# Kernel optimization log

Hardware: AMD Instinct MI355X
Metric: run time of the kernel (lower is better)

The kernel has to match this reference:

```python
import jax, jax.numpy as jnp
import numpy as np

N = 100_000   # nodes
E = 640_000   # edges
H = 128       # hidden_dim
L = 4         # num_layers
C = 2         # num_classes
G = 128       # graphs in batch

def setup_inputs() -> dict:
    key = jax.random.key(0)
    ks = jax.random.split(key, 8)
    x = jax.random.randint(ks[0], (N, 1), 0, 2)
    edge_index = jax.random.randint(ks[1], (2, E), 0, N)
    batch = jnp.sort(jax.random.randint(ks[2], (N,), 0, G))
    embed = jax.random.normal(ks[3], (2, H), jnp.float32)
    Ws = jax.random.normal(ks[4], (L, H, H), jnp.float32) * (1.0 / np.sqrt(H))
    bs = jnp.zeros((L, H), jnp.float32)
    W_out = jax.random.normal(ks[5], (H, C), jnp.float32) * (1.0 / np.sqrt(H))
    b_out = jnp.zeros((C,), jnp.float32)
    return dict(x=x, edge_index=edge_index, batch=batch, embed=embed,
                Ws=Ws, bs=bs, W_out=W_out, b_out=b_out)

def reference(x, edge_index, batch, embed, Ws, bs, W_out, b_out):
    src, dst = edge_index[0], edge_index[1]
    # symmetric GCN normalization with self-loops (PyG GCNConv default)
    deg = jax.ops.segment_sum(jnp.ones(E, jnp.float32), dst, num_segments=N) + 1.0
    dinv = jax.lax.rsqrt(deg)
    enorm = (dinv[src] * dinv[dst])[:, None]   # per-edge norm
    snorm = (dinv * dinv)[:, None]             # self-loop norm

    h = embed[x[:, 0]]                          # [N, H] embedding lookup
    n_layers = Ws.shape[0]
    for l in range(n_layers):
        t = h @ Ws[l]                           # linear transform [N, H]
        agg = jax.ops.segment_sum(t[src] * enorm, dst, num_segments=N) \
              + t * snorm + bs[l]
        h = jax.nn.relu(agg) if l < n_layers - 1 else agg

    # global mean pool over graph ids
    counts = jax.ops.segment_sum(jnp.ones(N, jnp.float32), batch, num_segments=G)
    pooled = jax.ops.segment_sum(h, batch, num_segments=G) \
             / jnp.maximum(counts, 1.0)[:, None]   # [G, H]
    return pooled @ W_out + b_out                  # [G, C]
```

## Files before the change

### kernel.cpp

```cpp
#include <hip/hip_runtime.h>

typedef __attribute__((ext_vector_type(8))) short bf16x8;
typedef __attribute__((ext_vector_type(4))) float f32x4;
typedef __attribute__((ext_vector_type(2))) float f32x2;

__device__ inline unsigned short bf16_rtn(float f) {
  unsigned u = __float_as_uint(f);
  unsigned r = u + 0x7fffu + ((u >> 16) & 1u);
  return (unsigned short)(r >> 16);
}

__device__ inline void split_bf16(float f, unsigned short& hi, unsigned short& lo) {
  hi = bf16_rtn(f);
  float fh = __uint_as_float((unsigned)hi << 16);
  lo = bf16_rtn(f - fh);
}

__device__ inline float bf16_to_f(unsigned short v) {
  return __uint_as_float((unsigned)v << 16);
}

__device__ inline unsigned char f_to_fp8(float f) {
  int r = __builtin_amdgcn_cvt_pk_fp8_f32(f, f, 0, false);
  return (unsigned char)(r & 0xff);
}
__device__ inline f32x2 fp8x2_to_f(unsigned short v) {
  return __builtin_amdgcn_cvt_pk_f32_fp8((int)v, false);
}

__global__ void k_init(int* __restrict__ deg, int* __restrict__ gpz, int N, int M,
                       const float* __restrict__ Ws, const float* __restrict__ embed,
                       unsigned short* __restrict__ wphi,
                       unsigned short* __restrict__ wplo,
                       float* __restrict__ T,
                       unsigned char* __restrict__ t_a,
                       unsigned char* __restrict__ t_b) {
  int i = blockIdx.x * 256 + threadIdx.x;
  if (i < N) deg[i] = 0;
  if (i < M) gpz[i] = 0;
  int l = blockIdx.x;
  if (l < 3) {
    const float* W = Ws + (size_t)(l + 1) * 128 * 128;
    unsigned short* dh = wphi + (size_t)l * 16384;
    unsigned short* dl = wplo + (size_t)l * 16384;
    for (int idx = threadIdx.x; idx < 16384; idx += 256) {
      int j = idx & 7;
      int lane = (idx >> 3) & 63;
      int c = (idx >> 9) & 3;
      int ct = idx >> 11;
      int k = c * 32 + ((lane >> 4) * 8) + j;
      int n = ct * 16 + (lane & 15);
      unsigned short hi, lo;
      split_bf16(W[k * 128 + n], hi, lo);
      dh[idx] = hi;
      dl[idx] = lo;
    }
  } else if (l == 3) {
    int t = threadIdx.x;
    int r = t >> 7, c = t & 127;
    float acc = 0.f;
    for (int k = 0; k < 128; ++k)
      acc += embed[r * 128 + k] * Ws[k * 128 + c];
    T[r * 128 + c] = acc;
  } else if (l == 4) {
    int t = threadIdx.x;
    if (t < 32)      ((unsigned*)(t_a + (size_t)N * 128))[t] = 0u;
    else if (t < 64) ((unsigned*)(t_b + (size_t)N * 128))[t - 32] = 0u;
  }
}


__global__ void k_hist(const int* __restrict__ dst, int* __restrict__ deg,
                       int* __restrict__ posr, int E) {
  int e = blockIdx.x * 256 + threadIdx.x;
  if (e < E) posr[e] = atomicAdd(&deg[dst[e]], 1);
}

__global__ void k_scan1(const int* __restrict__ deg, int* __restrict__ rowptr,
                        int* __restrict__ bsum, float* __restrict__ dpk,
                        const int* __restrict__ x, const int* __restrict__ batch,
                        int* __restrict__ gstart, int* __restrict__ gend, int N) {
  __shared__ int s[256];
  int t = threadIdx.x;
  int i = blockIdx.x * 256 + t;
  int v = (i < N) ? deg[i] : 0;
  if (i < N) {
    float di = rsqrtf((float)v + 1.0f);
    dpk[i] = x[i] ? -di : di;
    int g = batch[i];
    if (i == 0 || batch[i - 1] != g) gstart[g] = i;
    if (i == N - 1 || batch[i + 1] != g) gend[g] = i + 1;
  }
  s[t] = v;
  __syncthreads();
  for (int off = 1; off < 256; off <<= 1) {
    int u = (t >= off) ? s[t - off] : 0;
    __syncthreads();
    s[t] += u;
    __syncthreads();
  }
  if (i < N) rowptr[i] = s[t] - v;
  if (t == 255) bsum[blockIdx.x] = s[255];
}

__global__ void k_scan2(const int* __restrict__ bsum, int* __restrict__ boff, int nb) {
  __shared__ int s[512];
  int t = threadIdx.x;
  int v = (t < nb) ? bsum[t] : 0;
  s[t] = v;
  __syncthreads();
  for (int off = 1; off < 512; off <<= 1) {
    int u = (t >= off) ? s[t - off] : 0;
    __syncthreads();
    s[t] += u;
    __syncthreads();
  }
  boff[t] = s[t] - v;
}

__global__ void k_scan3(int* __restrict__ rowptr, const int* __restrict__ boff,
                        int N, int E) {
  int i = blockIdx.x * 256 + threadIdx.x;
  if (i < N) rowptr[i] += boff[i >> 8];
  if (i == 0) rowptr[N] = E;
}

__global__ void k_scatter(const int* __restrict__ src, const int* __restrict__ dst,
                          const int* __restrict__ posr, const int* __restrict__ rowptr,
                          const float* __restrict__ dpk,
                          int2* __restrict__ epack, int E) {
  int e = blockIdx.x * 256 + threadIdx.x;
  if (e >= E) return;
  int s = src[e], d = dst[e];
  int pos = rowptr[d] + posr[e];
  epack[pos] = make_int2(s, __float_as_int(dpk[s]));
}


__device__ inline void acc16(float* a, uint4 p) {
  f32x2 v;
  v = __builtin_amdgcn_cvt_pk_f32_fp8((int)p.x, false); a[0]  += v.x; a[1]  += v.y;
  v = __builtin_amdgcn_cvt_pk_f32_fp8((int)p.x, true);  a[2]  += v.x; a[3]  += v.y;
  v = __builtin_amdgcn_cvt_pk_f32_fp8((int)p.y, false); a[4]  += v.x; a[5]  += v.y;
  v = __builtin_amdgcn_cvt_pk_f32_fp8((int)p.y, true);  a[6]  += v.x; a[7]  += v.y;
  v = __builtin_amdgcn_cvt_pk_f32_fp8((int)p.z, false); a[8]  += v.x; a[9]  += v.y;
  v = __builtin_amdgcn_cvt_pk_f32_fp8((int)p.z, true);  a[10] += v.x; a[11] += v.y;
  v = __builtin_amdgcn_cvt_pk_f32_fp8((int)p.w, false); a[12] += v.x; a[13] += v.y;
  v = __builtin_amdgcn_cvt_pk_f32_fp8((int)p.w, true);  a[14] += v.x; a[15] += v.y;
}

__device__ inline void gather8(const unsigned char* __restrict__ tin,
                               const int2* __restrict__ epack,
                               int r0, int deg, int l8, int N,
                               float* a) {
  int dcap = deg < 16 ? deg : 16;
  int slo = N, shi = N;
  if (2 * l8 < dcap)     slo = epack[r0 + 2 * l8].x;
  if (2 * l8 + 1 < dcap) shi = epack[r0 + 2 * l8 + 1].x;

  uint4 p[16];
  #pragma unroll
  for (int k = 0; k < 8; ++k) {
    int se = __shfl(slo, k, 8);
    int so = __shfl(shi, k, 8);
    p[2 * k]     = *(const uint4*)(tin + (size_t)((unsigned)se * 128u + ((unsigned)l8 << 4)));
    p[2 * k + 1] = *(const uint4*)(tin + (size_t)((unsigned)so * 128u + ((unsigned)l8 << 4)));
  }
  #pragma unroll
  for (int k = 0; k < 16; ++k) acc16(a, p[k]);

  if (__builtin_expect(deg > 16, 0)) {
    for (int e = r0 + 16; e < r0 + deg; ++e) {
      int s = epack[e].x;
      uint4 q = *(const uint4*)(tin + (size_t)((unsigned)s * 128u + ((unsigned)l8 << 4)));
      acc16(a, q);
    }
  }
}

__global__ __launch_bounds__(256)
void k_agg(const unsigned char* __restrict__ tin,
           const int* __restrict__ rowptr,
           const int2* __restrict__ epack,
           const float* __restrict__ dpk, const float* __restrict__ bvec,
           unsigned short* __restrict__ h, int N) {
  int lane = threadIdx.x & 63;
  int g8 = lane >> 3, l8 = lane & 7;
  int wid = (blockIdx.x * 256 + threadIdx.x) >> 6;
  int i = wid * 8 + g8;
  if (i >= N) return;
  int r0 = rowptr[i], r1 = rowptr[i + 1];
  uint4 ps = *(const uint4*)(tin + (size_t)i * 128 + (l8 << 4));
  float dp = dpk[i];

  float a[16];
  #pragma unroll
  for (int k = 0; k < 16; ++k) a[k] = 0.f;
  gather8(tin, epack, r0, r1 - r0, l8, N, a);
  acc16(a, ps);

  float di = fabsf(dp);
  const float4* bp = (const float4*)(bvec + 16 * l8);
  float4 b0 = bp[0], b1 = bp[1], b2 = bp[2], b3 = bp[3];
  float bb[16] = {b0.x, b0.y, b0.z, b0.w, b1.x, b1.y, b1.z, b1.w,
                  b2.x, b2.y, b2.z, b2.w, b3.x, b3.y, b3.z, b3.w};
  unsigned u[8];
  #pragma unroll
  for (int k = 0; k < 8; ++k) {
    float v0 = fmaxf(di * a[2 * k]     + bb[2 * k],     0.f);
    float v1 = fmaxf(di * a[2 * k + 1] + bb[2 * k + 1], 0.f);
    u[k] = (unsigned)bf16_rtn(v0) | ((unsigned)bf16_rtn(v1) << 16);
  }
  uint4* hp = (uint4*)(h + (size_t)i * 128 + 16 * l8);
  hp[0] = make_uint4(u[0], u[1], u[2], u[3]);
  hp[1] = make_uint4(u[4], u[5], u[6], u[7]);
}

__global__ __launch_bounds__(256)
void k_agg_pool(const unsigned char* __restrict__ tin,
                const int* __restrict__ rowptr,
                const int2* __restrict__ epack,
                const float* __restrict__ dpk, const float* __restrict__ bvec,
                const int* __restrict__ batch,
                float* __restrict__ pooled, int N) {
  __shared__ float sh[32][128];
  __shared__ int sg[32];
  int lane = threadIdx.x & 63;
  int g8 = lane >> 3, l8 = lane & 7;
  int nloc = (threadIdx.x >> 6) * 8 + g8;
  int i = blockIdx.x * 32 + nloc;
  if (threadIdx.x < 32) sg[threadIdx.x] = -1;
  __syncthreads();
  if (i < N) {
    int r0 = rowptr[i], r1 = rowptr[i + 1];
    uint4 ps = *(const uint4*)(tin + (size_t)i * 128 + (l8 << 4));
    float dp = dpk[i];

    float a[16];
    #pragma unroll
    for (int k = 0; k < 16; ++k) a[k] = 0.f;
    gather8(tin, epack, r0, r1 - r0, l8, N, a);
    acc16(a, ps);

    float di = fabsf(dp);
    const float4* bp = (const float4*)(bvec + 16 * l8);
    float4 b0 = bp[0], b1 = bp[1], b2 = bp[2], b3 = bp[3];
    float bb[16] = {b0.x, b0.y, b0.z, b0.w, b1.x, b1.y, b1.z, b1.w,
                    b2.x, b2.y, b2.z, b2.w, b3.x, b3.y, b3.z, b3.w};
    #pragma unroll
    for (int k = 0; k < 16; ++k)
      sh[nloc][16 * l8 + k] = di * a[k] + bb[k];
    if (l8 == 0) sg[nloc] = batch[i];
  }
  __syncthreads();
  if (threadIdx.x < 128) {
    int c = threadIdx.x;
    float acc = 0.f;
    int cur = sg[0];
    #pragma unroll
    for (int w2 = 0; w2 < 32; ++w2) {
      int gw = sg[w2];
      if (gw < 0) break;
      if (gw != cur) {
        atomicAdd(&pooled[cur * 128 + c], acc);
        acc = 0.f;
        cur = gw;
      }
      acc += sh[w2][c];
    }
    atomicAdd(&pooled[cur * 128 + c], acc);
  }
}

__global__ void k_gemm(const unsigned short* __restrict__ h,
                       const unsigned short* __restrict__ wphi,
                       const unsigned short* __restrict__ wplo,
                       const float* __restrict__ dpk,
                       unsigned char* __restrict__ tout, int N) {
  int wave = threadIdx.x >> 6;
  int lane = threadIdx.x & 63;
  int r0 = (blockIdx.x * 4 + wave) * 32;
  if (r0 >= N) return;
  int q = lane >> 4;
  int m = lane & 15;
  const bf16x8* bh_base = (const bf16x8*)wphi;
  const bf16x8* bl_base = (const bf16x8*)wplo;

  f32x4 acc[2][8];
  #pragma unroll
  for (int tt = 0; tt < 2; ++tt)
    #pragma unroll
    for (int ct = 0; ct < 8; ++ct)
      acc[tt][ct] = (f32x4){0.f, 0.f, 0.f, 0.f};

  for (int c = 0; c < 4; ++c) {
    bf16x8 a0 = *(const bf16x8*)(h + (size_t)(r0 + m) * 128 + c * 32 + q * 8);
    bf16x8 a1 = *(const bf16x8*)(h + (size_t)(r0 + 16 + m) * 128 + c * 32 + q * 8);
    #pragma unroll
    for (int ct = 0; ct < 8; ++ct) {
      bf16x8 bh = bh_base[(ct * 4 + c) * 64 + lane];
      bf16x8 bl = bl_base[(ct * 4 + c) * 64 + lane];
      acc[0][ct] = __builtin_amdgcn_mfma_f32_16x16x32_bf16(a0, bh, acc[0][ct], 0, 0, 0);
      acc[0][ct] = __builtin_amdgcn_mfma_f32_16x16x32_bf16(a0, bl, acc[0][ct], 0, 0, 0);
      acc[1][ct] = __builtin_amdgcn_mfma_f32_16x16x32_bf16(a1, bh, acc[1][ct], 0, 0, 0);
      acc[1][ct] = __builtin_amdgcn_mfma_f32_16x16x32_bf16(a1, bl, acc[1][ct], 0, 0, 0);
    }
  }

  #pragma unroll
  for (int tt = 0; tt < 2; ++tt)
    #pragma unroll
    for (int ct = 0; ct < 8; ++ct)
      #pragma unroll
      for (int r = 0; r < 4; ++r) {
        int row = r0 + tt * 16 + q * 4 + r;
        if (row < N) {
          float sc = fabsf(dpk[row]);
          tout[(size_t)row * 128 + ct * 16 + m] = f_to_fp8(sc * acc[tt][ct][r]);
        }
      }
}

__device__ inline void gemm_tile8(const unsigned short* hT,
                                  const unsigned short* __restrict__ wphi,
                                  const unsigned short* __restrict__ wplo,
                                  const float* __restrict__ dpk,
                                  unsigned char* __restrict__ tout, int i0, int N) {
  int ct = threadIdx.x >> 6;
  int lane = threadIdx.x & 63;
  int q = lane >> 4;
  int m = lane & 15;
  const bf16x8* bh_base = (const bf16x8*)wphi;
  const bf16x8* bl_base = (const bf16x8*)wplo;

  f32x4 acc0 = (f32x4){0.f, 0.f, 0.f, 0.f};
  f32x4 acc1 = (f32x4){0.f, 0.f, 0.f, 0.f};

  #pragma unroll
  for (int c = 0; c < 4; ++c) {
    bf16x8 a0 = *(const bf16x8*)(hT + (m) * 136 + c * 32 + q * 8);
    bf16x8 a1 = *(const bf16x8*)(hT + (16 + m) * 136 + c * 32 + q * 8);
    bf16x8 bh = bh_base[(ct * 4 + c) * 64 + lane];
    bf16x8 bl = bl_base[(ct * 4 + c) * 64 + lane];
    acc0 = __builtin_amdgcn_mfma_f32_16x16x32_bf16(a0, bh, acc0, 0, 0, 0);
    acc0 = __builtin_amdgcn_mfma_f32_16x16x32_bf16(a0, bl, acc0, 0, 0, 0);
    acc1 = __builtin_amdgcn_mfma_f32_16x16x32_bf16(a1, bh, acc1, 0, 0, 0);
    acc1 = __builtin_amdgcn_mfma_f32_16x16x32_bf16(a1, bl, acc1, 0, 0, 0);
  }

  #pragma unroll
  for (int r = 0; r < 4; ++r) {
    int row0 = i0 + q * 4 + r;
    int row1 = row0 + 16;
    if (row0 < N) {
      float sc = fabsf(dpk[row0]);
      tout[(size_t)row0 * 128 + ct * 16 + m] = f_to_fp8(sc * acc0[r]);
    }
    if (row1 < N) {
      float sc = fabsf(dpk[row1]);
      tout[(size_t)row1 * 128 + ct * 16 + m] = f_to_fp8(sc * acc1[r]);
    }
  }
}

__global__ __launch_bounds__(512)
void k_l1_gemm(const int* __restrict__ rowptr,
               const int2* __restrict__ epack,
               const float* __restrict__ dpk, const float* __restrict__ T,
               const float* __restrict__ b0,
               const unsigned short* __restrict__ wphi,
               const unsigned short* __restrict__ wplo,
               unsigned char* __restrict__ tout, int N) {
  __shared__ unsigned short hT[32 * 136];
  int wave = threadIdx.x >> 6;
  int lane = threadIdx.x & 63;
  int i0 = blockIdx.x * 32;

  for (int j = wave * 4; j < wave * 4 + 4; ++j) {
    int i = i0 + j;
    if (i >= N) break;
    int r0 = rowptr[i], r1 = rowptr[i + 1];
    float sabs = 0.f, sneg = 0.f;
    for (int e = r0 + lane; e < r1; e += 64) {
      float wv = __int_as_float(epack[e].y);
      float aw = fabsf(wv);
      sabs += aw;
      if (wv < 0.f) sneg += aw;
    }
    for (int mm = 32; mm >= 1; mm >>= 1) {
      sabs += __shfl_xor(sabs, mm, 64);
      sneg += __shfl_xor(sneg, mm, 64);
    }
    float dp = dpk[i];
    float di = fabsf(dp);
    float sn = di * di;
    float c1 = di * sneg;
    float c0 = di * (sabs - sneg);
    if (dp < 0.f) c1 += sn; else c0 += sn;
    float v0 = fmaxf(c0 * T[2 * lane]     + c1 * T[128 + 2 * lane]     + b0[2 * lane],     0.f);
    float v1 = fmaxf(c0 * T[2 * lane + 1] + c1 * T[128 + 2 * lane + 1] + b0[2 * lane + 1], 0.f);
    *(unsigned*)&hT[j * 136 + 2 * lane] = (unsigned)bf16_rtn(v0) | ((unsigned)bf16_rtn(v1) << 16);
  }
  __syncthreads();
  gemm_tile8(hT, wphi, wplo, dpk, tout, i0, N);
}

__global__ void k_out(const float* __restrict__ pooled, const int* __restrict__ gstart,
                      const int* __restrict__ gend, const float* __restrict__ W_out,
                      const float* __restrict__ b_out, float* __restrict__ out, int G) {
  __shared__ float sp[128];
  int g = blockIdx.x;
  int j = threadIdx.x;
  float cnt = (float)(gend[g] - gstart[g]);
  sp[j] = pooled[g * 128 + j] / fmaxf(cnt, 1.f);
  __syncthreads();
  if (j < 2) {
    float o = b_out[j];
    for (int k = 0; k < 128; ++k)
      o += sp[k] * W_out[k * 2 + j];
    out[g * 2 + j] = o;
  }
}

extern "C" void kernel_launch(void* const* d_in, const int* in_sizes, int n_in,
                              void* d_out, int out_size, void* d_ws, size_t ws_size,
                              hipStream_t stream) {
  const int*   x     = (const int*)d_in[0];
  const int*   ei    = (const int*)d_in[1];
  const int*   batch = (const int*)d_in[2];
  const float* embed = (const float*)d_in[3];
  const float* Ws    = (const float*)d_in[4];
  const float* bs    = (const float*)d_in[5];
  const float* W_out = (const float*)d_in[6];
  const float* b_out = (const float*)d_in[7];
  float* out = (float*)d_out;

  int N = in_sizes[2];
  int E = in_sizes[1] / 2;
  int G = out_size / 2;

  const int* src = ei;
  const int* dst = ei + E;

  char* w = (char*)d_ws;
  auto alloc = [&](size_t bytes) {
    char* p = w;
    w += (bytes + 255) & ~(size_t)255;
    return p;
  };
  int*   deg    = (int*)  alloc((size_t)N * 4);
  float* dpk    = (float*)alloc((size_t)N * 4);
  int*   rowptr = (int*)  alloc((size_t)(N + 1) * 4);
  int*   posr   = (int*)  alloc((size_t)E * 4);
  int*   bsum   = (int*)  alloc(512 * 4);
  int*   boff   = (int*)  alloc(512 * 4);
  int*   gstart = (int*)  alloc((size_t)G * 4);
  int*   gend   = (int*)  alloc((size_t)G * 4);
  float* pooled = (float*)alloc((size_t)G * 128 * 4);
  float* T      = (float*)alloc(256 * 4);
  unsigned short* wphi = (unsigned short*)alloc((size_t)3 * 16384 * 2);
  unsigned short* wplo = (unsigned short*)alloc((size_t)3 * 16384 * 2);
  int2*  epack  = (int2*) alloc((size_t)E * 8);
  unsigned short* h = (unsigned short*)alloc((size_t)N * 128 * 2);
  unsigned char* t_a = (unsigned char*)alloc((size_t)(N + 1) * 128);
  unsigned char* t_b = (unsigned char*)alloc((size_t)(N + 1) * 128);

  int nbN = (N + 255) / 256;
  int nbE = (E + 255) / 256;
  int ntile = (N + 31) / 32;
  int nagg = (N + 31) / 32;
  int ngemm = (N + 127) / 128;
  int M = G * 130;

  k_init<<<nbN, 256, 0, stream>>>(deg, gstart, N, M, Ws, embed, wphi, wplo, T, t_a, t_b);
  k_hist<<<nbE, 256, 0, stream>>>(dst, deg, posr, E);
  k_scan1<<<nbN, 256, 0, stream>>>(deg, rowptr, bsum, dpk, x, batch, gstart, gend, N);
  k_scan2<<<1, 512, 0, stream>>>(bsum, boff, nbN);
  k_scan3<<<nbN, 256, 0, stream>>>(rowptr, boff, N, E);
  k_scatter<<<nbE, 256, 0, stream>>>(src, dst, posr, rowptr, dpk, epack, E);

  k_l1_gemm<<<ntile, 512, 0, stream>>>(rowptr, epack, dpk, T, bs,
                                       wphi, wplo, t_a, N);
  k_agg<<<nagg, 256, 0, stream>>>(t_a, rowptr, epack, dpk, bs + 128, h, N);
  k_gemm<<<ngemm, 256, 0, stream>>>(h, wphi + 16384, wplo + 16384, dpk, t_b, N);
  k_agg<<<nagg, 256, 0, stream>>>(t_b, rowptr, epack, dpk, bs + 256, h, N);
  k_gemm<<<ngemm, 256, 0, stream>>>(h, wphi + 32768, wplo + 32768, dpk, t_a, N);
  k_agg_pool<<<nagg, 256, 0, stream>>>(t_a, rowptr, epack, dpk, bs + 384,
                                       batch, pooled, N);
  k_out<<<G, 128, 0, stream>>>(pooled, gstart, gend, W_out, b_out, out, G);
}
```

Baseline: 288.1 us.

## Shrink edge list to src-only, merge scan kernels, stage GEMM rows in LDS

Measured after the change: 314.1 us. 1.09x slower.

```diff
diff --git a/kernel.cpp b/kernel.cpp
--- a/kernel.cpp
+++ b/kernel.cpp
@@ -16,16 +16,9 @@
   lo = bf16_rtn(f - fh);
 }
 
-__device__ inline float bf16_to_f(unsigned short v) {
-  return __uint_as_float((unsigned)v << 16);
-}
-
 __device__ inline unsigned char f_to_fp8(float f) {
   int r = __builtin_amdgcn_cvt_pk_fp8_f32(f, f, 0, false);
   return (unsigned char)(r & 0xff);
-}
-__device__ inline f32x2 fp8x2_to_f(unsigned short v) {
-  return __builtin_amdgcn_cvt_pk_f32_fp8((int)v, false);
 }
 
 __global__ void k_init(int* __restrict__ deg, int* __restrict__ gpz, int N, int M,
@@ -103,37 +96,31 @@
   if (t == 255) bsum[blockIdx.x] = s[255];
 }
 
-__global__ void k_scan2(const int* __restrict__ bsum, int* __restrict__ boff, int nb) {
-  __shared__ int s[512];
-  int t = threadIdx.x;
-  int v = (t < nb) ? bsum[t] : 0;
-  s[t] = v;
-  __syncthreads();
-  for (int off = 1; off < 512; off <<= 1) {
-    int u = (t >= off) ? s[t - off] : 0;
+__global__ void k_scanB(int* __restrict__ rowptr, const int* __restrict__ bsum,
+                        int N, int E) {
+  __shared__ int red[256];
+  int b = blockIdx.x, t = threadIdx.x;
+  int s = 0;
+  for (int j = t; j < b; j += 256) s += bsum[j];
+  red[t] = s;
+  __syncthreads();
+  for (int off = 128; off >= 1; off >>= 1) {
+    if (t < off) red[t] += red[t + off];
     __syncthreads();
-    s[t] += u;
-    __syncthreads();
-  }
-  boff[t] = s[t] - v;
-}
-
-__global__ void k_scan3(int* __restrict__ rowptr, const int* __restrict__ boff,
-                        int N, int E) {
-  int i = blockIdx.x * 256 + threadIdx.x;
-  if (i < N) rowptr[i] += boff[i >> 8];
+  }
+  int boff = red[0];
+  int i = b * 256 + t;
+  if (i < N) rowptr[i] += boff;
   if (i == 0) rowptr[N] = E;
 }
 
 __global__ void k_scatter(const int* __restrict__ src, const int* __restrict__ dst,
                           const int* __restrict__ posr, const int* __restrict__ rowptr,
-                          const float* __restrict__ dpk,
-                          int2* __restrict__ epack, int E) {
+                          int* __restrict__ esrc, int E) {
   int e = blockIdx.x * 256 + threadIdx.x;
   if (e >= E) return;
-  int s = src[e], d = dst[e];
-  int pos = rowptr[d] + posr[e];
-  epack[pos] = make_int2(s, __float_as_int(dpk[s]));
+  int d = dst[e];
+  esrc[rowptr[d] + posr[e]] = src[e];
 }
 
 
@@ -150,13 +137,13 @@
 }
 
 __device__ inline void gather8(const unsigned char* __restrict__ tin,
-                               const int2* __restrict__ epack,
+                               const int* __restrict__ esrc,
                                int r0, int deg, int l8, int N,
                                float* a) {
   int dcap = deg < 16 ? deg : 16;
   int slo = N, shi = N;
-  if (2 * l8 < dcap)     slo = epack[r0 + 2 * l8].x;
-  if (2 * l8 + 1 < dcap) shi = epack[r0 + 2 * l8 + 1].x;
+  if (2 * l8 < dcap)     slo = esrc[r0 + 2 * l8];
+  if (2 * l8 + 1 < dcap) shi = esrc[r0 + 2 * l8 + 1];
 
   uint4 p[16];
   #pragma unroll
@@ -171,7 +158,7 @@
 
   if (__builtin_expect(deg > 16, 0)) {
     for (int e = r0 + 16; e < r0 + deg; ++e) {
-      int s = epack[e].x;
+      int s = esrc[e];
       uint4 q = *(const uint4*)(tin + (size_t)((unsigned)s * 128u + ((unsigned)l8 << 4)));
       acc16(a, q);
     }
@@ -181,7 +168,7 @@
 __global__ __launch_bounds__(256)
 void k_agg(const unsigned char* __restrict__ tin,
            const int* __restrict__ rowptr,
-           const int2* __restrict__ epack,
+           const int* __restrict__ esrc,
            const float* __restrict__ dpk, const float* __restrict__ bvec,
            unsigned short* __restrict__ h, int N) {
   int lane = threadIdx.x & 63;
@@ -196,7 +183,7 @@
   float a[16];
   #pragma unroll
   for (int k = 0; k < 16; ++k) a[k] = 0.f;
-  gather8(tin, epack, r0, r1 - r0, l8, N, a);
+  gather8(tin, esrc, r0, r1 - r0, l8, N, a);
   acc16(a, ps);
 
   float di = fabsf(dp);
@@ -219,7 +206,7 @@
 __global__ __launch_bounds__(256)
 void k_agg_pool(const unsigned char* __restrict__ tin,
                 const int* __restrict__ rowptr,
-                const int2* __restrict__ epack,
+                const int* __restrict__ esrc,
                 const float* __restrict__ dpk, const float* __restrict__ bvec,
                 const int* __restrict__ batch,
                 float* __restrict__ pooled, int N) {
@@ -239,7 +226,7 @@
     float a[16];
     #pragma unroll
     for (int k = 0; k < 16; ++k) a[k] = 0.f;
-    gather8(tin, epack, r0, r1 - r0, l8, N, a);
+    gather8(tin, esrc, r0, r1 - r0, l8, N, a);
     acc16(a, ps);
 
     float di = fabsf(dp);
@@ -272,17 +259,34 @@
   }
 }
 
-__global__ void k_gemm(const unsigned short* __restrict__ h,
-                       const unsigned short* __restrict__ wphi,
-                       const unsigned short* __restrict__ wplo,
-                       const float* __restrict__ dpk,
-                       unsigned char* __restrict__ tout, int N) {
-  int wave = threadIdx.x >> 6;
-  int lane = threadIdx.x & 63;
-  int r0 = (blockIdx.x * 4 + wave) * 32;
-  if (r0 >= N) return;
+__global__ __launch_bounds__(256)
+void k_gemm(const unsigned short* __restrict__ h,
+            const unsigned short* __restrict__ wphi,
+            const unsigned short* __restrict__ wplo,
+            const float* __restrict__ dpk,
+            unsigned char* __restrict__ tout, int N) {
+  __shared__ unsigned short hT[128 * 136];
+  int i0 = blockIdx.x * 128;
+  int t = threadIdx.x;
+
+  #pragma unroll
+  for (int k = 0; k < 8; ++k) {
+    int idx = t + k * 256;
+    int row = idx >> 4, col16 = idx & 15;
+    uint4 v = make_uint4(0u, 0u, 0u, 0u);
+    if (i0 + row < N)
+      v = *(const uint4*)(h + (size_t)(i0 + row) * 128 + col16 * 8);
+    *(uint4*)&hT[row * 136 + col16 * 8] = v;
+  }
+  __syncthreads();
+
+  int wave = t >> 6;
+  int lane = t & 63;
   int q = lane >> 4;
   int m = lane & 15;
+  int r0 = i0 + wave * 32;
+  if (r0 >= N) return;
+  const unsigned short* hw = hT + (wave * 32) * 136;
   const bf16x8* bh_base = (const bf16x8*)wphi;
   const bf16x8* bl_base = (const bf16x8*)wplo;
 
@@ -293,9 +297,10 @@
     for (int ct = 0; ct < 8; ++ct)
       acc[tt][ct] = (f32x4){0.f, 0.f, 0.f, 0.f};
 
+  #pragma unroll
   for (int c = 0; c < 4; ++c) {
-    bf16x8 a0 = *(const bf16x8*)(h + (size_t)(r0 + m) * 128 + c * 32 + q * 8);
-    bf16x8 a1 = *(const bf16x8*)(h + (size_t)(r0 + 16 + m) * 128 + c * 32 + q * 8);
+    bf16x8 a0 = *(const bf16x8*)(hw + m * 136 + c * 32 + q * 8);
+    bf16x8 a1 = *(const bf16x8*)(hw + (16 + m) * 136 + c * 32 + q * 8);
     #pragma unroll
     for (int ct = 0; ct < 8; ++ct) {
       bf16x8 bh = bh_base[(ct * 4 + c) * 64 + lane];
@@ -365,7 +370,7 @@
 
 __global__ __launch_bounds__(512)
 void k_l1_gemm(const int* __restrict__ rowptr,
-               const int2* __restrict__ epack,
+               const int* __restrict__ esrc,
                const float* __restrict__ dpk, const float* __restrict__ T,
                const float* __restrict__ b0,
                const unsigned short* __restrict__ wphi,
@@ -382,7 +387,7 @@
     int r0 = rowptr[i], r1 = rowptr[i + 1];
     float sabs = 0.f, sneg = 0.f;
     for (int e = r0 + lane; e < r1; e += 64) {
-      float wv = __int_as_float(epack[e].y);
+      float wv = dpk[esrc[e]];
       float aw = fabsf(wv);
       sabs += aw;
       if (wv < 0.f) sneg += aw;
@@ -453,14 +458,13 @@
   int*   rowptr = (int*)  alloc((size_t)(N + 1) * 4);
   int*   posr   = (int*)  alloc((size_t)E * 4);
   int*   bsum   = (int*)  alloc(512 * 4);
-  int*   boff   = (int*)  alloc(512 * 4);
   int*   gstart = (int*)  alloc((size_t)G * 4);
   int*   gend   = (int*)  alloc((size_t)G * 4);
   float* pooled = (float*)alloc((size_t)G * 128 * 4);
   float* T      = (float*)alloc(256 * 4);
   unsigned short* wphi = (unsigned short*)alloc((size_t)3 * 16384 * 2);
   unsigned short* wplo = (unsigned short*)alloc((size_t)3 * 16384 * 2);
-  int2*  epack  = (int2*) alloc((size_t)E * 8);
+  int*   esrc   = (int*)  alloc((size_t)(E + 16) * 4);
   unsigned short* h = (unsigned short*)alloc((size_t)N * 128 * 2);
   unsigned char* t_a = (unsigned char*)alloc((size_t)(N + 1) * 128);
   unsigned char* t_b = (unsigned char*)alloc((size_t)(N + 1) * 128);
@@ -475,17 +479,16 @@
   k_init<<<nbN, 256, 0, stream>>>(deg, gstart, N, M, Ws, embed, wphi, wplo, T, t_a, t_b);
   k_hist<<<nbE, 256, 0, stream>>>(dst, deg, posr, E);
   k_scan1<<<nbN, 256, 0, stream>>>(deg, rowptr, bsum, dpk, x, batch, gstart, gend, N);
-  k_scan2<<<1, 512, 0, stream>>>(bsum, boff, nbN);
-  k_scan3<<<nbN, 256, 0, stream>>>(rowptr, boff, N, E);
-  k_scatter<<<nbE, 256, 0, stream>>>(src, dst, posr, rowptr, dpk, epack, E);
-
-  k_l1_gemm<<<ntile, 512, 0, stream>>>(rowptr, epack, dpk, T, bs,
+  k_scanB<<<nbN, 256, 0, stream>>>(rowptr, bsum, N, E);
+  k_scatter<<<nbE, 256, 0, stream>>>(src, dst, posr, rowptr, esrc, E);
+
+  k_l1_gemm<<<ntile, 512, 0, stream>>>(rowptr, esrc, dpk, T, bs,
                                        wphi, wplo, t_a, N);
-  k_agg<<<nagg, 256, 0, stream>>>(t_a, rowptr, epack, dpk, bs + 128, h, N);
+  k_agg<<<nagg, 256, 0, stream>>>(t_a, rowptr, esrc, dpk, bs + 128, h, N);
   k_gemm<<<ngemm, 256, 0, stream>>>(h, wphi + 16384, wplo + 16384, dpk, t_b, N);
-  k_agg<<<nagg, 256, 0, stream>>>(t_b, rowptr, epack, dpk, bs + 256, h, N);
+  k_agg<<<nagg, 256, 0, stream>>>(t_b, rowptr, esrc, dpk, bs + 256, h, N);
   k_gemm<<<ngemm, 256, 0, stream>>>(h, wphi + 32768, wplo + 32768, dpk, t_a, N);
-  k_agg_pool<<<nagg, 256, 0, stream>>>(t_a, rowptr, epack, dpk, bs + 384,
+  k_agg_pool<<<nagg, 256, 0, stream>>>(t_a, rowptr, esrc, dpk, bs + 384,
                                        batch, pooled, N);
   k_out<<<G, 128, 0, stream>>>(pooled, gstart, gend, W_out, b_out, out, G);
 }
```
